# Kernel optimization log

Hardware: AMD Instinct MI355X
Metric: run time of the kernel (lower is better)

Reference implementation:

```python
import jax, jax.numpy as jnp
import numpy as np

B, T, N, IN_DIM, H = 8, 16, 1024, 2, 128
HEADS, HD = 8, 16            # HEADS*HD == H (DGL GATConv head-concat)
SNP, SEQ_OUT, DEG = 4, 12, 8
NT = SNP * N                 # nodes per HSTG graph
CKPNT = [4, 7, 10, 13, 16]   # _generate_checkpoints(4, 16)
LRELU = 0.2


def _build_edges():
    # HSTG: per-snapshot spatial edges (random deg-8 adjacency + self-loops)
    # plus identity temporal edges t -> t+1 (uni-direction, non-dense, sync).
    rng = np.random.default_rng(0)
    src, dst = [], []
    ar = np.arange(N)
    for t in range(SNP):
        off = t * N
        src.append(rng.integers(0, N, size=N * DEG) + off)
        dst.append(np.repeat(ar, DEG) + off)
        src.append(ar + off)   # self-loops (keep every dst non-empty)
        dst.append(ar + off)
    for t in range(SNP - 1):
        src.append(ar + t * N)
        dst.append(ar + (t + 1) * N)
    return (jnp.asarray(np.concatenate(src), dtype=jnp.int32),
            jnp.asarray(np.concatenate(dst), dtype=jnp.int32))


def setup_inputs() -> dict:
    key = jax.random.key(0)
    ks = jax.random.split(key, 16)
    edge_src, edge_dst = _build_edges()
    rn = lambda k, s, sc: jax.random.normal(k, s, dtype=jnp.float32) * sc
    return {
        'inputs': rn(ks[0], (B, T, N, IN_DIM), 1.0),
        'W_in': rn(ks[1], (IN_DIM, H), 0.5),
        'b_in': jnp.zeros((H,), jnp.float32),
        'spatial_emb': rn(ks[2], (N, H), 0.05),
        'temporal_emb': rn(ks[3], (N, T), 0.05),
        'gat_w0': rn(ks[4], (H, HEADS * HD), 0.1),
        'gat_al0': rn(ks[5], (HEADS, HD), 0.1),
        'gat_ar0': rn(ks[6], (HEADS, HD), 0.1),
        'gat_b0': jnp.zeros((HEADS * HD,), jnp.float32),
        'gat_w1': rn(ks[7], (H, HEADS * HD), 0.1),
        'gat_al1': rn(ks[8], (HEADS, HD), 0.1),
        'gat_ar1': rn(ks[9], (HEADS, HD), 0.1),
        'gat_b1': jnp.zeros((HEADS * HD,), jnp.float32),
        'agg_q': rn(ks[10], (N, H), 0.1),
        'w_out1': rn(ks[11], (1, SEQ_OUT), 0.5),
        'b_out1': jnp.zeros((SEQ_OUT,), jnp.float32),
        'w_out2': rn(ks[12], (H, 1), 0.1),
        'b_out2': jnp.zeros((1,), jnp.float32),
        'edge_src': edge_src,
        'edge_dst': edge_dst,
    }


def _gat_layer(x, W, a_l, a_r, b, src, dst, activate):
    # x: [NT, H] node features of one graph
    feat = (x @ W).reshape(NT, HEADS, HD)
    el = jnp.sum(feat * a_l, axis=-1)                 # [NT, HEADS]
    er = jnp.sum(feat * a_r, axis=-1)
    e = jax.nn.leaky_relu(el[src] + er[dst], LRELU)    # [E, HEADS]
    m = jax.ops.segment_max(e, dst, num_segments=NT)
    w = jnp.exp(e - m[dst])
    s = jax.ops.segment_sum(w, dst, num_segments=NT)
    alpha = w / s[dst]
    out = jax.ops.segment_sum(feat[src] * alpha[..., None], dst, num_segments=NT)
    out = out.reshape(NT, HEADS * HD) + b
    return jax.nn.elu(out) if activate else out


def reference(inputs, W_in, b_in, spatial_emb, temporal_emb,
              gat_w0, gat_al0, gat_ar0, gat_b0,
              gat_w1, gat_al1, gat_ar1, gat_b1,
              agg_q, w_out1, b_out1, w_out2, b_out2,
              edge_src, edge_dst):
    # input projection + spatial/temporal embeddings
    x = inputs @ W_in + b_in                           # [B,T,N,H]
    x = x + spatial_emb                                # broadcast [N,H]
    x = x + temporal_emb.T[None, :, :, None]           # add temb[n,t] at [b,t,n,h]

    def gat(xb):  # xb: [NT,H], one sample of the batched block-diagonal graph
        h = _gat_layer(xb, gat_w0, gat_al0, gat_ar0, gat_b0, edge_src, edge_dst, True)
        return _gat_layer(h, gat_w1, gat_al1, gat_ar1, gat_b1, edge_src, edge_dst, False)
    gat_b = jax.vmap(gat)

    last = None
    left = 0
    for idx, right in enumerate(CKPNT):
        fs = x[:, left:right]                          # [B, snp or snp-1, N, H]
        if idx != 0:
            fs = jnp.concatenate([last, fs], axis=1)   # [B, SNP, N, H]
        residual = fs
        h = gat_b(fs.reshape(B, NT, H)).reshape(B, SNP, N, H)
        h = h + residual
        # Aggregator: per-node attention over the SNP snapshots -> [B,1,N,H]
        scores = jnp.einsum('btnh,nh->btn', h, agg_q)
        alpha = jax.nn.softmax(scores, axis=1)
        last = jnp.einsum('btn,btnh->bnh', alpha, h)[:, None]
        # LayerNorm over normalized_shape [1,N,H], no affine
        mu = jnp.mean(last, axis=(1, 2, 3), keepdims=True)
        var = jnp.var(last, axis=(1, 2, 3), keepdims=True)
        last = (last - mu) * jax.lax.rsqrt(var + 1e-5)
        left = right

    # decoder (meta_decode = False)
    t = jnp.transpose(last, (0, 3, 2, 1))              # [B,H,N,1]
    o = jax.nn.relu(t @ w_out1 + b_out1)               # [B,H,N,SEQ_OUT]
    o = jnp.transpose(o, (0, 3, 2, 1))                 # [B,SEQ_OUT,N,H]
    return o @ w_out2 + b_out2                         # [B,SEQ_OUT,N,1]
```

## Files before the change

kernel.cpp:

```cpp
#include <hip/hip_runtime.h>
#include <hip/hip_bf16.h>
#include <math.h>

constexpr int kB = 8;
constexpr int kT = 16;
constexpr int kN = 1024;
constexpr int kH = 128;
constexpr int kSNP = 4;
constexpr int kNT = kSNP * kN;
constexpr int kRows = kB * kNT;
constexpr int kSeqOut = 12;
constexpr float kLRelu = 0.2f;
constexpr int kEdgePerSnap = kN * 8 + kN;
constexpr int kSelfOff = kN * 8;
constexpr int kTempBase = kSNP * kEdgePerSnap;
constexpr int kStatsPerIter = kB * 8 * 16;

typedef __bf16 bf16x8 __attribute__((ext_vector_type(8)));
typedef float f32x4 __attribute__((ext_vector_type(4)));

__global__ void build_fs(const float* __restrict__ inputs, const float* __restrict__ W_in,
                         const float* __restrict__ b_in, const float* __restrict__ spatial,
                         const float* __restrict__ temporal, const float* __restrict__ last,
                         const float* __restrict__ stats, float* __restrict__ A,
                         int left, int first) {
  int blk = blockIdx.x;
  int b = blk & 7;
  int inner = blk >> 3;
  int idx4 = (b << 17) | (inner << 8) | threadIdx.x;
  int h4 = idx4 & 31;
  int n  = (idx4 >> 5) & 1023;
  int t  = (idx4 >> 15) & 3;
  float4 out;
  if (!first && t == 0) {
    float s1 = 0.f, s2 = 0.f;
    #pragma unroll
    for (int s = 0; s < 8; ++s) {
      s1 += stats[b * 128 + s * 16];
      s2 += stats[b * 128 + s * 16 + 1];
    }
    const float inv = 1.0f / (float)(kN * kH);
    float mu = s1 * inv;
    float var = s2 * inv - mu * mu;
    float sc = rsqrtf(var + 1e-5f);
    float4 v = *(const float4*)(last + ((size_t)(b * kN + n)) * kH + h4 * 4);
    out.x = (v.x - mu) * sc; out.y = (v.y - mu) * sc;
    out.z = (v.z - mu) * sc; out.w = (v.w - mu) * sc;
  } else {
    int tg = left + t - (first ? 0 : 1);
    float2 iv = *(const float2*)(inputs + ((size_t)((b * kT + tg) * kN + n)) * 2);
    float tv = temporal[n * kT + tg];
    float4 w0 = *(const float4*)(W_in + h4 * 4);
    float4 w1 = *(const float4*)(W_in + kH + h4 * 4);
    float4 bb = *(const float4*)(b_in + h4 * 4);
    float4 sp = *(const float4*)(spatial + n * kH + h4 * 4);
    out.x = iv.x * w0.x + iv.y * w1.x + bb.x + sp.x + tv;
    out.y = iv.x * w0.y + iv.y * w1.y + bb.y + sp.y + tv;
    out.z = iv.x * w0.z + iv.y * w1.z + bb.z + sp.z + tv;
    out.w = iv.x * w0.w + iv.y * w1.w + bb.w + sp.w + tv;
  }
  *(float4*)(A + (size_t)idx4 * 4) = out;
}

__launch_bounds__(256)
__global__ void gemm_mfma(const float* __restrict__ In, const float* __restrict__ W,
                          const float* __restrict__ gal, const float* __restrict__ gar,
                          float* __restrict__ Out, float* __restrict__ elp,
                          float* __restrict__ erp) {
  __shared__ unsigned short AhL[64 * 128];
  __shared__ unsigned short AlL[64 * 128];
  int tid = threadIdx.x;
  int lane = tid & 63, wid = tid >> 6;
  int blk = blockIdx.x;
  int rowblk = ((blk & 7) << 6) | (blk >> 3);
  int blockRow0 = rowblk * 64;

  union BU { unsigned short u[8]; bf16x8 v; };
  BU bh[2][4], bl[2][4];
  int colL = lane & 15;
  int kgrp = (lane >> 4) * 8;
  #pragma unroll
  for (int c = 0; c < 2; ++c) {
    int col = wid * 32 + c * 16 + colL;
    #pragma unroll
    for (int s = 0; s < 4; ++s) {
      #pragma unroll
      for (int j = 0; j < 8; ++j) {
        int k = s * 32 + kgrp + j;
        float w = W[k * kH + col];
        unsigned int bits = __float_as_uint(w);
        bh[c][s].u[j] = (unsigned short)(bits >> 16);
        float hif = __uint_as_float(bits & 0xffff0000u);
        bl[c][s].u[j] = (unsigned short)(__float_as_uint(w - hif) >> 16);
      }
    }
  }

  const float* Ablk = In + (size_t)blockRow0 * kH;
  #pragma unroll
  for (int itn = 0; itn < 8; ++itn) {
    int fid = itn * 256 + tid;
    int row = fid >> 5, kq = fid & 31;
    float4 v = *(const float4*)(Ablk + (size_t)row * kH + kq * 4);
    ushort4 hi, lo;
    unsigned int bx = __float_as_uint(v.x);
    hi.x = bx >> 16; lo.x = __float_as_uint(v.x - __uint_as_float(bx & 0xffff0000u)) >> 16;
    unsigned int by = __float_as_uint(v.y);
    hi.y = by >> 16; lo.y = __float_as_uint(v.y - __uint_as_float(by & 0xffff0000u)) >> 16;
    unsigned int bz = __float_as_uint(v.z);
    hi.z = bz >> 16; lo.z = __float_as_uint(v.z - __uint_as_float(bz & 0xffff0000u)) >> 16;
    unsigned int bw = __float_as_uint(v.w);
    hi.w = bw >> 16; lo.w = __float_as_uint(v.w - __uint_as_float(bw & 0xffff0000u)) >> 16;
    int boff = (row * 256 + kq * 8) ^ ((row & 7) << 4);
    *(ushort4*)((char*)AhL + boff) = hi;
    *(ushort4*)((char*)AlL + boff) = lo;
  }
  __syncthreads();

  f32x4 acc[4][2];
  #pragma unroll
  for (int rb = 0; rb < 4; ++rb)
    #pragma unroll
    for (int c = 0; c < 2; ++c) acc[rb][c] = (f32x4){0.f, 0.f, 0.f, 0.f};

  #pragma unroll
  for (int s = 0; s < 4; ++s) {
    bf16x8 ah[4], alr[4];
    #pragma unroll
    for (int rb = 0; rb < 4; ++rb) {
      int row = rb * 16 + colL;
      int boff = (row * 256 + s * 64 + (lane >> 4) * 16) ^ ((row & 7) << 4);
      ah[rb]  = *(const bf16x8*)((const char*)AhL + boff);
      alr[rb] = *(const bf16x8*)((const char*)AlL + boff);
    }
    #pragma unroll
    for (int c = 0; c < 2; ++c) {
      #pragma unroll
      for (int rb = 0; rb < 4; ++rb)
        acc[rb][c] = __builtin_amdgcn_mfma_f32_16x16x32_bf16(ah[rb], bh[c][s].v, acc[rb][c], 0, 0, 0);
      #pragma unroll
      for (int rb = 0; rb < 4; ++rb)
        acc[rb][c] = __builtin_amdgcn_mfma_f32_16x16x32_bf16(alr[rb], bh[c][s].v, acc[rb][c], 0, 0, 0);
      #pragma unroll
      for (int rb = 0; rb < 4; ++rb)
        acc[rb][c] = __builtin_amdgcn_mfma_f32_16x16x32_bf16(ah[rb], bl[c][s].v, acc[rb][c], 0, 0, 0);
    }
  }

  int rquad = (lane >> 4) * 4;
  #pragma unroll
  for (int c = 0; c < 2; ++c) {
    int h = wid * 2 + c;
    float alv = gal[h * 16 + colL];
    float arv = gar[h * 16 + colL];
    int col = wid * 32 + c * 16 + colL;
    #pragma unroll
    for (int rb = 0; rb < 4; ++rb) {
      f32x4 a = acc[rb][c];
      int row0g = blockRow0 + rb * 16 + rquad;
      #pragma unroll
      for (int r = 0; r < 4; ++r)
        Out[(size_t)(row0g + r) * kH + col] = a[r];
      float e0 = a[0] * alv, e1 = a[1] * alv, e2 = a[2] * alv, e3 = a[3] * alv;
      float f0 = a[0] * arv, f1 = a[1] * arv, f2 = a[2] * arv, f3 = a[3] * arv;
      #pragma unroll
      for (int m = 1; m < 16; m <<= 1) {
        e0 += __shfl_xor(e0, m, 64); e1 += __shfl_xor(e1, m, 64);
        e2 += __shfl_xor(e2, m, 64); e3 += __shfl_xor(e3, m, 64);
        f0 += __shfl_xor(f0, m, 64); f1 += __shfl_xor(f1, m, 64);
        f2 += __shfl_xor(f2, m, 64); f3 += __shfl_xor(f3, m, 64);
      }
      if (colL == 0) {
        elp[(size_t)(row0g + 0) * 8 + h] = e0;
        elp[(size_t)(row0g + 1) * 8 + h] = e1;
        elp[(size_t)(row0g + 2) * 8 + h] = e2;
        elp[(size_t)(row0g + 3) * 8 + h] = e3;
        erp[(size_t)(row0g + 0) * 8 + h] = f0;
        erp[(size_t)(row0g + 1) * 8 + h] = f1;
        erp[(size_t)(row0g + 2) * 8 + h] = f2;
        erp[(size_t)(row0g + 3) * 8 + h] = f3;
      }
    }
  }
}

template <int LAYER>
__launch_bounds__(256)
__global__ void agg_kernel(const float* __restrict__ feat, const float* __restrict__ el,
                           const float* __restrict__ er, const int* __restrict__ esrc,
                           const float* __restrict__ bias, const float* __restrict__ resid,
                           float* __restrict__ outp) {
  int blk = blockIdx.x;
  int b = blk & 7;
  int inner = blk >> 3;
  int tid = threadIdx.x;
  int v = inner * 16 + (tid >> 4);
  int h2 = tid & 15;
  int h = h2 >> 1;
  int t = v >> 10;
  int n = v & 1023;
  int bv = (b << 12) + v;

  int srcs[10];
  int base8 = t * kEdgePerSnap + n * 8;
  #pragma unroll
  for (int k = 0; k < 8; ++k) srcs[k] = esrc[base8 + k];
  srcs[8] = esrc[t * kEdgePerSnap + kSelfOff + n];
  float erv = er[bv * 8 + h];
  int ebase = b << 15;

  float e[10];
  float m = -1e30f;
  #pragma unroll
  for (int i = 0; i < 9; ++i) {
    float x = el[ebase + srcs[i] * 8 + h] + erv;
    x = x > 0.f ? x : kLRelu * x;
    e[i] = x;
    m = fmaxf(m, x);
  }
  if (t > 0) {
    int s9 = esrc[kTempBase + (t - 1) * kN + n];
    srcs[9] = s9;
    float x = el[ebase + s9 * 8 + h] + erv;
    x = x > 0.f ? x : kLRelu * x;
    e[9] = x;
    m = fmaxf(m, x);
  } else {
    srcs[9] = v;
    e[9] = -1e30f;
  }
  float s = 0.f;
  #pragma unroll
  for (int i = 0; i < 10; ++i) { e[i] = expf(e[i] - m); s += e[i]; }
  float inv = 1.0f / s;

  float4 acc0 = {0,0,0,0}, acc1 = {0,0,0,0};
  size_t fbase = (size_t)(b << 12) * kH;
  #pragma unroll
  for (int i = 0; i < 10; ++i) {
    float w = e[i] * inv;
    const float4* fp = (const float4*)(feat + fbase + (size_t)srcs[i] * kH + h2 * 8);
    float4 v0 = fp[0], v1 = fp[1];
    acc0.x += w * v0.x; acc0.y += w * v0.y; acc0.z += w * v0.z; acc0.w += w * v0.w;
    acc1.x += w * v1.x; acc1.y += w * v1.y; acc1.z += w * v1.z; acc1.w += w * v1.w;
  }
  size_t ob = (size_t)bv * kH + h2 * 8;
  const float4* bb = (const float4*)(bias + h2 * 8);
  float4 accs[2] = {acc0, acc1};
  #pragma unroll
  for (int j = 0; j < 2; ++j) {
    float4 a = accs[j], bj = bb[j];
    float4 o;
    if (LAYER == 0) {
      float x0 = a.x + bj.x, x1 = a.y + bj.y, x2 = a.z + bj.z, x3 = a.w + bj.w;
      o.x = x0 > 0.f ? x0 : expm1f(x0);
      o.y = x1 > 0.f ? x1 : expm1f(x1);
      o.z = x2 > 0.f ? x2 : expm1f(x2);
      o.w = x3 > 0.f ? x3 : expm1f(x3);
    } else {
      float4 r = *(const float4*)(resid + ob + j * 4);
      o.x = a.x + bj.x + r.x; o.y = a.y + bj.y + r.y;
      o.z = a.z + bj.z + r.z; o.w = a.w + bj.w + r.w;
    }
    *(float4*)(outp + ob + j * 4) = o;
  }
}

__global__ void attn_kernel(const float* __restrict__ hbuf, const float* __restrict__ q,
                            float* __restrict__ last, float* __restrict__ stats) {
  __shared__ float sred[8];
  int tid = threadIdx.x;
  int wave = tid >> 6, lane = tid & 63;
  int blk = blockIdx.x;
  int b = blk & 7;
  int inner = blk >> 3;
  int d0 = lane * 2;
  float p1 = 0.f, p2 = 0.f;
  for (int i = 0; i < 4; ++i) {
    int n = inner * 16 + wave * 4 + i;
    float2 qv = *(const float2*)(q + (size_t)n * kH + d0);
    float2 hv[4];
    float sc[4];
    #pragma unroll
    for (int t = 0; t < 4; ++t) {
      hv[t] = *(const float2*)(hbuf + ((size_t)(b * kNT + t * kN + n)) * kH + d0);
      float p = hv[t].x * qv.x + hv[t].y * qv.y;
      #pragma unroll
      for (int s = 1; s < 64; s <<= 1) p += __shfl_xor(p, s, 64);
      sc[t] = p;
    }
    float m = fmaxf(fmaxf(sc[0], sc[1]), fmaxf(sc[2], sc[3]));
    float a0 = expf(sc[0] - m), a1 = expf(sc[1] - m);
    float a2 = expf(sc[2] - m), a3 = expf(sc[3] - m);
    float id = 1.0f / (a0 + a1 + a2 + a3);
    float lx = (a0 * hv[0].x + a1 * hv[1].x + a2 * hv[2].x + a3 * hv[3].x) * id;
    float ly = (a0 * hv[0].y + a1 * hv[1].y + a2 * hv[2].y + a3 * hv[3].y) * id;
    float2 lo = {lx, ly};
    *(float2*)(last + ((size_t)(b * kN + n)) * kH + d0) = lo;
    p1 += lx + ly;
    p2 += lx * lx + ly * ly;
  }
  #pragma unroll
  for (int s = 1; s < 64; s <<= 1) {
    p1 += __shfl_xor(p1, s, 64);
    p2 += __shfl_xor(p2, s, 64);
  }
  if (lane == 0) { sred[wave * 2] = p1; sred[wave * 2 + 1] = p2; }
  __syncthreads();
  if (tid == 0) {
    int slot = inner & 7;
    atomicAdd(&stats[b * 128 + slot * 16],     sred[0] + sred[2] + sred[4] + sred[6]);
    atomicAdd(&stats[b * 128 + slot * 16 + 1], sred[1] + sred[3] + sred[5] + sred[7]);
  }
}

__global__ void out_kernel(const float* __restrict__ last, const float* __restrict__ stats,
                           const float* __restrict__ w1, const float* __restrict__ b1,
                           const float* __restrict__ w2, const float* __restrict__ b2,
                           float* __restrict__ out) {
  int tid = threadIdx.x;
  int wave = tid >> 6, lane = tid & 63;
  int gw = blockIdx.x * 4 + wave;
  int b = gw >> 10, n = gw & 1023;
  float s1 = 0.f, s2 = 0.f;
  #pragma unroll
  for (int s = 0; s < 8; ++s) {
    s1 += stats[b * 128 + s * 16];
    s2 += stats[b * 128 + s * 16 + 1];
  }
  const float inv = 1.0f / (float)(kN * kH);
  float mu = s1 * inv;
  float var = s2 * inv - mu * mu;
  float scv = rsqrtf(var + 1e-5f);
  int d0 = lane * 2;
  float2 lv = *(const float2*)(last + ((size_t)(b * kN + n)) * kH + d0);
  float x0 = (lv.x - mu) * scv, x1 = (lv.y - mu) * scv;
  float w20 = w2[d0], w21 = w2[d0 + 1];
  float bias2 = b2[0];
  #pragma unroll
  for (int s = 0; s < kSeqOut; ++s) {
    float w1s = w1[s], b1s = b1[s];
    float v = fmaxf(x0 * w1s + b1s, 0.f) * w20 + fmaxf(x1 * w1s + b1s, 0.f) * w21;
    #pragma unroll
    for (int k = 1; k < 64; k <<= 1) v += __shfl_xor(v, k, 64);
    if (lane == 0) out[(size_t)(b * kSeqOut + s) * kN + n] = v + bias2;
  }
}

extern "C" void kernel_launch(void* const* d_in, const int* in_sizes, int n_in,
                              void* d_out, int out_size, void* d_ws, size_t ws_size,
                              hipStream_t stream) {
  const float* inputs   = (const float*)d_in[0];
  const float* W_in     = (const float*)d_in[1];
  const float* b_in     = (const float*)d_in[2];
  const float* spatial  = (const float*)d_in[3];
  const float* temporal = (const float*)d_in[4];
  const float* gw0      = (const float*)d_in[5];
  const float* gal0     = (const float*)d_in[6];
  const float* gar0     = (const float*)d_in[7];
  const float* gb0      = (const float*)d_in[8];
  const float* gw1      = (const float*)d_in[9];
  const float* gal1     = (const float*)d_in[10];
  const float* gar1     = (const float*)d_in[11];
  const float* gb1      = (const float*)d_in[12];
  const float* aggq     = (const float*)d_in[13];
  const float* w_out1   = (const float*)d_in[14];
  const float* b_out1   = (const float*)d_in[15];
  const float* w_out2   = (const float*)d_in[16];
  const float* b_out2   = (const float*)d_in[17];
  const int*   esrc     = (const int*)d_in[18];

  float* ws = (float*)d_ws;
  float* A     = ws;
  float* Bf    = ws + 4194304;
  float* C     = ws + 8388608;
  float* el    = ws + 12582912;
  float* er    = ws + 12845056;
  float* last  = ws + 13107200;
  float* stats = ws + 14155776;

  hipMemsetAsync(stats, 0, 5 * kStatsPerIter * sizeof(float), stream);

  const int lefts[5] = {0, 4, 7, 10, 13};
  for (int it = 0; it < 5; ++it) {
    const float* st_prev = (it == 0) ? stats : (stats + (it - 1) * kStatsPerIter);
    build_fs<<<4096, 256, 0, stream>>>(inputs, W_in, b_in, spatial, temporal,
                                       last, st_prev, A, lefts[it], it == 0 ? 1 : 0);
    gemm_mfma<<<kRows / 64, 256, 0, stream>>>(A, gw0, gal0, gar0, Bf, el, er);
    agg_kernel<0><<<2048, 256, 0, stream>>>(Bf, el, er, esrc, gb0, nullptr, C);
    gemm_mfma<<<kRows / 64, 256, 0, stream>>>(C, gw1, gal1, gar1, Bf, el, er);
    agg_kernel<1><<<2048, 256, 0, stream>>>(Bf, el, er, esrc, gb1, A, C);
    attn_kernel<<<512, 256, 0, stream>>>(C, aggq, last, stats + it * kStatsPerIter);
  }
  out_kernel<<<2048, 256, 0, stream>>>(last, stats + 4 * kStatsPerIter, w_out1, b_out1,
                                       w_out2, b_out2, (float*)d_out);
}
```

Before: 487.3 us.

## Pre-split GAT weights once, remap aggregation threads, fuse layer-1 agg with attention

Adds a one-time prep kernel that splits both GAT weight matrices into bf16 hi/lo parts in MFMA fragment order, so the GEMM loads packed vectors instead of converting fp32 weights in every block. The aggregation kernels are remapped to one wave per node with float2 per lane. The second-layer aggregation is fused with the snapshot attention/softmax and LayerNorm stats, which removes a separate kernel and the round trip of the layer output through global memory. The stats slot count doubles to 16 per batch to spread the atomics, but the fused kernel uses more blocks, runs two block barriers and leaves half its threads idle in the final reduction.

After: 510.0 us. +4.7%, slower.

```diff
diff --git a/kernel.cpp b/kernel.cpp
--- a/kernel.cpp
+++ b/kernel.cpp
@@ -14,10 +14,28 @@
 constexpr int kEdgePerSnap = kN * 8 + kN;
 constexpr int kSelfOff = kN * 8;
 constexpr int kTempBase = kSNP * kEdgePerSnap;
-constexpr int kStatsPerIter = kB * 8 * 16;
+constexpr int kStatsPerIter = kB * 16 * 16;
 
 typedef __bf16 bf16x8 __attribute__((ext_vector_type(8)));
 typedef float f32x4 __attribute__((ext_vector_type(4)));
+
+__global__ void prep_w(const float* __restrict__ gw0, const float* __restrict__ gw1,
+                       unsigned short* __restrict__ wbuf) {
+  int tid = blockIdx.x * 256 + threadIdx.x;
+  int layer = tid >> 14;
+  int e = tid & 16383;
+  int k = e >> 7, col = e & 127;
+  const float* W = layer ? gw1 : gw0;
+  float w = W[k * kH + col];
+  unsigned int bits = __float_as_uint(w);
+  unsigned short hi = (unsigned short)(bits >> 16);
+  float hif = __uint_as_float(bits & 0xffff0000u);
+  unsigned short lo = (unsigned short)(__float_as_uint(w - hif) >> 16);
+  int s = k >> 5, q = (k >> 3) & 3, j = k & 7;
+  int off = ((s * 4 + q) * kH + col) * 8 + j;
+  wbuf[layer * 32768 + off] = hi;
+  wbuf[layer * 32768 + 16384 + off] = lo;
+}
 
 __global__ void build_fs(const float* __restrict__ inputs, const float* __restrict__ W_in,
                          const float* __restrict__ b_in, const float* __restrict__ spatial,
@@ -35,9 +53,9 @@
   if (!first && t == 0) {
     float s1 = 0.f, s2 = 0.f;
     #pragma unroll
-    for (int s = 0; s < 8; ++s) {
-      s1 += stats[b * 128 + s * 16];
-      s2 += stats[b * 128 + s * 16 + 1];
+    for (int s = 0; s < 16; ++s) {
+      s1 += stats[b * 256 + s * 16];
+      s2 += stats[b * 256 + s * 16 + 1];
     }
     const float inv = 1.0f / (float)(kN * kH);
     float mu = s1 * inv;
@@ -63,7 +81,8 @@
 }
 
 __launch_bounds__(256)
-__global__ void gemm_mfma(const float* __restrict__ In, const float* __restrict__ W,
+__global__ void gemm_mfma(const float* __restrict__ In, const unsigned short* __restrict__ Wh,
+                          const unsigned short* __restrict__ Wl,
                           const float* __restrict__ gal, const float* __restrict__ gar,
                           float* __restrict__ Out, float* __restrict__ elp,
                           float* __restrict__ erp) {
@@ -74,25 +93,18 @@
   int blk = blockIdx.x;
   int rowblk = ((blk & 7) << 6) | (blk >> 3);
   int blockRow0 = rowblk * 64;
-
-  union BU { unsigned short u[8]; bf16x8 v; };
-  BU bh[2][4], bl[2][4];
   int colL = lane & 15;
-  int kgrp = (lane >> 4) * 8;
+  int q = lane >> 4;
+
+  bf16x8 bh[2][4], bl[2][4];
   #pragma unroll
   for (int c = 0; c < 2; ++c) {
     int col = wid * 32 + c * 16 + colL;
     #pragma unroll
     for (int s = 0; s < 4; ++s) {
-      #pragma unroll
-      for (int j = 0; j < 8; ++j) {
-        int k = s * 32 + kgrp + j;
-        float w = W[k * kH + col];
-        unsigned int bits = __float_as_uint(w);
-        bh[c][s].u[j] = (unsigned short)(bits >> 16);
-        float hif = __uint_as_float(bits & 0xffff0000u);
-        bl[c][s].u[j] = (unsigned short)(__float_as_uint(w - hif) >> 16);
-      }
+      int off = ((s * 4 + q) * kH + col) * 8;
+      bh[c][s] = *(const bf16x8*)(Wh + off);
+      bl[c][s] = *(const bf16x8*)(Wl + off);
     }
   }
 
@@ -129,7 +141,7 @@
     #pragma unroll
     for (int rb = 0; rb < 4; ++rb) {
       int row = rb * 16 + colL;
-      int boff = (row * 256 + s * 64 + (lane >> 4) * 16) ^ ((row & 7) << 4);
+      int boff = (row * 256 + s * 64 + q * 16) ^ ((row & 7) << 4);
       ah[rb]  = *(const bf16x8*)((const char*)AhL + boff);
       alr[rb] = *(const bf16x8*)((const char*)AlL + boff);
     }
@@ -137,17 +149,17 @@
     for (int c = 0; c < 2; ++c) {
       #pragma unroll
       for (int rb = 0; rb < 4; ++rb)
-        acc[rb][c] = __builtin_amdgcn_mfma_f32_16x16x32_bf16(ah[rb], bh[c][s].v, acc[rb][c], 0, 0, 0);
+        acc[rb][c] = __builtin_amdgcn_mfma_f32_16x16x32_bf16(ah[rb], bh[c][s], acc[rb][c], 0, 0, 0);
       #pragma unroll
       for (int rb = 0; rb < 4; ++rb)
-        acc[rb][c] = __builtin_amdgcn_mfma_f32_16x16x32_bf16(alr[rb], bh[c][s].v, acc[rb][c], 0, 0, 0);
+        acc[rb][c] = __builtin_amdgcn_mfma_f32_16x16x32_bf16(alr[rb], bh[c][s], acc[rb][c], 0, 0, 0);
       #pragma unroll
       for (int rb = 0; rb < 4; ++rb)
-        acc[rb][c] = __builtin_amdgcn_mfma_f32_16x16x32_bf16(ah[rb], bl[c][s].v, acc[rb][c], 0, 0, 0);
+        acc[rb][c] = __builtin_amdgcn_mfma_f32_16x16x32_bf16(ah[rb], bl[c][s], acc[rb][c], 0, 0, 0);
     }
   }
 
-  int rquad = (lane >> 4) * 4;
+  int rquad = q * 4;
   #pragma unroll
   for (int c = 0; c < 2; ++c) {
     int h = wid * 2 + c;
@@ -184,21 +196,18 @@
   }
 }
 
-template <int LAYER>
 __launch_bounds__(256)
-__global__ void agg_kernel(const float* __restrict__ feat, const float* __restrict__ el,
-                           const float* __restrict__ er, const int* __restrict__ esrc,
-                           const float* __restrict__ bias, const float* __restrict__ resid,
-                           float* __restrict__ outp) {
+__global__ void agg0_kernel(const float* __restrict__ feat, const float* __restrict__ el,
+                            const float* __restrict__ er, const int* __restrict__ esrc,
+                            const float* __restrict__ bias, float* __restrict__ outp) {
   int blk = blockIdx.x;
   int b = blk & 7;
-  int inner = blk >> 3;
+  int grp = blk >> 3;
   int tid = threadIdx.x;
-  int v = inner * 16 + (tid >> 4);
-  int h2 = tid & 15;
-  int h = h2 >> 1;
-  int t = v >> 10;
-  int n = v & 1023;
+  int wave = tid >> 6, lane = tid & 63;
+  int v = grp * 4 + wave;
+  int t = v >> 10, n = v & 1023;
+  int h = lane >> 3;
   int bv = (b << 12) + v;
 
   int srcs[10];
@@ -234,83 +243,122 @@
   for (int i = 0; i < 10; ++i) { e[i] = expf(e[i] - m); s += e[i]; }
   float inv = 1.0f / s;
 
-  float4 acc0 = {0,0,0,0}, acc1 = {0,0,0,0};
+  float ax = 0.f, ay = 0.f;
   size_t fbase = (size_t)(b << 12) * kH;
   #pragma unroll
   for (int i = 0; i < 10; ++i) {
     float w = e[i] * inv;
-    const float4* fp = (const float4*)(feat + fbase + (size_t)srcs[i] * kH + h2 * 8);
-    float4 v0 = fp[0], v1 = fp[1];
-    acc0.x += w * v0.x; acc0.y += w * v0.y; acc0.z += w * v0.z; acc0.w += w * v0.w;
-    acc1.x += w * v1.x; acc1.y += w * v1.y; acc1.z += w * v1.z; acc1.w += w * v1.w;
-  }
-  size_t ob = (size_t)bv * kH + h2 * 8;
-  const float4* bb = (const float4*)(bias + h2 * 8);
-  float4 accs[2] = {acc0, acc1};
-  #pragma unroll
-  for (int j = 0; j < 2; ++j) {
-    float4 a = accs[j], bj = bb[j];
-    float4 o;
-    if (LAYER == 0) {
-      float x0 = a.x + bj.x, x1 = a.y + bj.y, x2 = a.z + bj.z, x3 = a.w + bj.w;
-      o.x = x0 > 0.f ? x0 : expm1f(x0);
-      o.y = x1 > 0.f ? x1 : expm1f(x1);
-      o.z = x2 > 0.f ? x2 : expm1f(x2);
-      o.w = x3 > 0.f ? x3 : expm1f(x3);
-    } else {
-      float4 r = *(const float4*)(resid + ob + j * 4);
-      o.x = a.x + bj.x + r.x; o.y = a.y + bj.y + r.y;
-      o.z = a.z + bj.z + r.z; o.w = a.w + bj.w + r.w;
-    }
-    *(float4*)(outp + ob + j * 4) = o;
-  }
-}
-
-__global__ void attn_kernel(const float* __restrict__ hbuf, const float* __restrict__ q,
-                            float* __restrict__ last, float* __restrict__ stats) {
-  __shared__ float sred[8];
-  int tid = threadIdx.x;
-  int wave = tid >> 6, lane = tid & 63;
+    float2 fv = *(const float2*)(feat + fbase + (size_t)srcs[i] * kH + lane * 2);
+    ax += w * fv.x;
+    ay += w * fv.y;
+  }
+  float2 bb = *(const float2*)(bias + lane * 2);
+  float x0 = ax + bb.x, x1 = ay + bb.y;
+  float2 o;
+  o.x = x0 > 0.f ? x0 : expm1f(x0);
+  o.y = x1 > 0.f ? x1 : expm1f(x1);
+  *(float2*)(outp + (size_t)bv * kH + lane * 2) = o;
+}
+
+__launch_bounds__(256)
+__global__ void agg1_attn(const float* __restrict__ feat, const float* __restrict__ el,
+                          const float* __restrict__ er, const int* __restrict__ esrc,
+                          const float* __restrict__ bias, const float* __restrict__ resid,
+                          const float* __restrict__ q, float* __restrict__ last,
+                          float* __restrict__ stats) {
+  __shared__ float ssc[4];
+  __shared__ float hbuf[4][128];
+  __shared__ float sred[4];
   int blk = blockIdx.x;
   int b = blk & 7;
-  int inner = blk >> 3;
-  int d0 = lane * 2;
+  int n = blk >> 3;
+  int tid = threadIdx.x;
+  int t = tid >> 6, lane = tid & 63;
+  int v = (t << 10) + n;
+  int h = lane >> 3;
+  int bv = (b << 12) + v;
+
+  int srcs[10];
+  int base8 = t * kEdgePerSnap + n * 8;
+  #pragma unroll
+  for (int k = 0; k < 8; ++k) srcs[k] = esrc[base8 + k];
+  srcs[8] = esrc[t * kEdgePerSnap + kSelfOff + n];
+  float erv = er[bv * 8 + h];
+  int ebase = b << 15;
+
+  float e[10];
+  float m = -1e30f;
+  #pragma unroll
+  for (int i = 0; i < 9; ++i) {
+    float x = el[ebase + srcs[i] * 8 + h] + erv;
+    x = x > 0.f ? x : kLRelu * x;
+    e[i] = x;
+    m = fmaxf(m, x);
+  }
+  if (t > 0) {
+    int s9 = esrc[kTempBase + (t - 1) * kN + n];
+    srcs[9] = s9;
+    float x = el[ebase + s9 * 8 + h] + erv;
+    x = x > 0.f ? x : kLRelu * x;
+    e[9] = x;
+    m = fmaxf(m, x);
+  } else {
+    srcs[9] = v;
+    e[9] = -1e30f;
+  }
+  float s = 0.f;
+  #pragma unroll
+  for (int i = 0; i < 10; ++i) { e[i] = expf(e[i] - m); s += e[i]; }
+  float inv = 1.0f / s;
+
+  float ax = 0.f, ay = 0.f;
+  size_t fbase = (size_t)(b << 12) * kH;
+  #pragma unroll
+  for (int i = 0; i < 10; ++i) {
+    float w = e[i] * inv;
+    float2 fv = *(const float2*)(feat + fbase + (size_t)srcs[i] * kH + lane * 2);
+    ax += w * fv.x;
+    ay += w * fv.y;
+  }
+  float2 bb = *(const float2*)(bias + lane * 2);
+  float2 rv = *(const float2*)(resid + (size_t)bv * kH + lane * 2);
+  float hx = ax + bb.x + rv.x;
+  float hy = ay + bb.y + rv.y;
+
+  float2 qv = *(const float2*)(q + (size_t)n * kH + lane * 2);
+  float p = hx * qv.x + hy * qv.y;
+  #pragma unroll
+  for (int s_ = 1; s_ < 64; s_ <<= 1) p += __shfl_xor(p, s_, 64);
+  if (lane == 0) ssc[t] = p;
+  __syncthreads();
+  float s0 = ssc[0], s1 = ssc[1], s2 = ssc[2], s3 = ssc[3];
+  float mm = fmaxf(fmaxf(s0, s1), fmaxf(s2, s3));
+  float a0 = expf(s0 - mm), a1 = expf(s1 - mm), a2 = expf(s2 - mm), a3 = expf(s3 - mm);
+  float denom = 1.0f / (a0 + a1 + a2 + a3);
+  float at = (t == 0 ? a0 : t == 1 ? a1 : t == 2 ? a2 : a3) * denom;
+  hbuf[t][lane * 2]     = hx * at;
+  hbuf[t][lane * 2 + 1] = hy * at;
+  __syncthreads();
+
   float p1 = 0.f, p2 = 0.f;
-  for (int i = 0; i < 4; ++i) {
-    int n = inner * 16 + wave * 4 + i;
-    float2 qv = *(const float2*)(q + (size_t)n * kH + d0);
-    float2 hv[4];
-    float sc[4];
-    #pragma unroll
-    for (int t = 0; t < 4; ++t) {
-      hv[t] = *(const float2*)(hbuf + ((size_t)(b * kNT + t * kN + n)) * kH + d0);
-      float p = hv[t].x * qv.x + hv[t].y * qv.y;
-      #pragma unroll
-      for (int s = 1; s < 64; s <<= 1) p += __shfl_xor(p, s, 64);
-      sc[t] = p;
-    }
-    float m = fmaxf(fmaxf(sc[0], sc[1]), fmaxf(sc[2], sc[3]));
-    float a0 = expf(sc[0] - m), a1 = expf(sc[1] - m);
-    float a2 = expf(sc[2] - m), a3 = expf(sc[3] - m);
-    float id = 1.0f / (a0 + a1 + a2 + a3);
-    float lx = (a0 * hv[0].x + a1 * hv[1].x + a2 * hv[2].x + a3 * hv[3].x) * id;
-    float ly = (a0 * hv[0].y + a1 * hv[1].y + a2 * hv[2].y + a3 * hv[3].y) * id;
-    float2 lo = {lx, ly};
-    *(float2*)(last + ((size_t)(b * kN + n)) * kH + d0) = lo;
-    p1 += lx + ly;
-    p2 += lx * lx + ly * ly;
-  }
-  #pragma unroll
-  for (int s = 1; s < 64; s <<= 1) {
-    p1 += __shfl_xor(p1, s, 64);
-    p2 += __shfl_xor(p2, s, 64);
-  }
-  if (lane == 0) { sred[wave * 2] = p1; sred[wave * 2 + 1] = p2; }
+  if (tid < 128) {
+    int d = tid;
+    float sum = hbuf[0][d] + hbuf[1][d] + hbuf[2][d] + hbuf[3][d];
+    last[((size_t)(b * kN + n)) * kH + d] = sum;
+    p1 = sum;
+    p2 = sum * sum;
+  }
+  #pragma unroll
+  for (int s_ = 1; s_ < 64; s_ <<= 1) {
+    p1 += __shfl_xor(p1, s_, 64);
+    p2 += __shfl_xor(p2, s_, 64);
+  }
+  if (tid < 128 && lane == 0) { sred[t * 2] = p1; sred[t * 2 + 1] = p2; }
   __syncthreads();
   if (tid == 0) {
-    int slot = inner & 7;
-    atomicAdd(&stats[b * 128 + slot * 16],     sred[0] + sred[2] + sred[4] + sred[6]);
-    atomicAdd(&stats[b * 128 + slot * 16 + 1], sred[1] + sred[3] + sred[5] + sred[7]);
+    int slot = n & 15;
+    atomicAdd(&stats[b * 256 + slot * 16],     sred[0] + sred[2]);
+    atomicAdd(&stats[b * 256 + slot * 16 + 1], sred[1] + sred[3]);
   }
 }
 
@@ -324,9 +372,9 @@
   int b = gw >> 10, n = gw & 1023;
   float s1 = 0.f, s2 = 0.f;
   #pragma unroll
-  for (int s = 0; s < 8; ++s) {
-    s1 += stats[b * 128 + s * 16];
-    s2 += stats[b * 128 + s * 16 + 1];
+  for (int s = 0; s < 16; ++s) {
+    s1 += stats[b * 256 + s * 16];
+    s2 += stats[b * 256 + s * 16 + 1];
   }
   const float inv = 1.0f / (float)(kN * kH);
   float mu = s1 * inv;
@@ -378,19 +426,25 @@
   float* er    = ws + 12845056;
   float* last  = ws + 13107200;
   float* stats = ws + 14155776;
+  unsigned short* wsplit = (unsigned short*)(ws + 14166016);
 
   hipMemsetAsync(stats, 0, 5 * kStatsPerIter * sizeof(float), stream);
+  prep_w<<<128, 256, 0, stream>>>(gw0, gw1, wsplit);
+  const unsigned short* w0h = wsplit;
+  const unsigned short* w0l = wsplit + 16384;
+  const unsigned short* w1h = wsplit + 32768;
+  const unsigned short* w1l = wsplit + 49152;
 
   const int lefts[5] = {0, 4, 7, 10, 13};
   for (int it = 0; it < 5; ++it) {
     const float* st_prev = (it == 0) ? stats : (stats + (it - 1) * kStatsPerIter);
     build_fs<<<4096, 256, 0, stream>>>(inputs, W_in, b_in, spatial, temporal,
                                        last, st_prev, A, lefts[it], it == 0 ? 1 : 0);
-    gemm_mfma<<<kRows / 64, 256, 0, stream>>>(A, gw0, gal0, gar0, Bf, el, er);
-    agg_kernel<0><<<2048, 256, 0, stream>>>(Bf, el, er, esrc, gb0, nullptr, C);
-    gemm_mfma<<<kRows / 64, 256, 0, stream>>>(C, gw1, gal1, gar1, Bf, el, er);
-    agg_kernel<1><<<2048, 256, 0, stream>>>(Bf, el, er, esrc, gb1, A, C);
-    attn_kernel<<<512, 256, 0, stream>>>(C, aggq, last, stats + it * kStatsPerIter);
+    gemm_mfma<<<kRows / 64, 256, 0, stream>>>(A, w0h, w0l, gal0, gar0, Bf, el, er);
+    agg0_kernel<<<8192, 256, 0, stream>>>(Bf, el, er, esrc, gb0, C);
+    gemm_mfma<<<kRows / 64, 256, 0, stream>>>(C, w1h, w1l, gal1, gar1, Bf, el, er);
+    agg1_attn<<<8192, 256, 0, stream>>>(Bf, el, er, esrc, gb1, A, aggq, last,
+                                        stats + it * kStatsPerIter);
   }
   out_kernel<<<2048, 256, 0, stream>>>(last, stats + 4 * kStatsPerIter, w_out1, b_out1,
                                        w_out2, b_out2, (float*)d_out);
```
